# Kernel tuning notes

Hardware: AMD Instinct MI355X
Metric: run time of the kernel (lower is better)

Reference implementation:

```python
import jax, jax.numpy as jnp
import numpy as np

E = 512   # embed_dim
H = 8     # num_heads
B = 64    # num graphs
N = 255   # nodes per graph (equal counts -> padded mask is all-true)


def setup_inputs() -> dict:
    key = jax.random.key(0)
    ks = jax.random.split(key, 12)
    x = jax.random.normal(ks[0], (B * N, E), jnp.float32)
    metal_x = jax.random.normal(ks[1], (B, E), jnp.float32)
    batch = jnp.repeat(jnp.arange(B, dtype=jnp.int32), N)
    s = 1.0 / np.sqrt(E)
    def u(k, shape):
        return jax.random.uniform(k, shape, jnp.float32, -s, s)
    return {
        "x": x, "metal_x": metal_x, "batch": batch,
        "Wq": u(ks[2], (E, E)), "Wk": u(ks[3], (E, E)), "Wv": u(ks[4], (E, E)),
        "bq": u(ks[5], (E,)), "bk": u(ks[6], (E,)), "bv": u(ks[7], (E,)),
        "Wo": u(ks[8], (E, E)), "bo": u(ks[9], (E,)),
    }


def reference(x, metal_x, batch, Wq, Wk, Wv, bq, bk, bv, Wo, bo):
    # batch is sorted with equal per-graph counts, so the torch
    # pad_sequence([cat(metal_x[i], x[batch==i])]) construction is exactly a
    # reshape + concat, and key_padding_mask (~mask) is all-False.
    nb, e = metal_x.shape
    n = x.shape[0] // nb
    L = n + 1
    dh = e // H
    # value: [B, L, E] with the metal token at position 0
    value = jnp.concatenate([metal_x[:, None, :], x.reshape(nb, n, e)], axis=1)
    # key/query_sequential are identity; torch MHA in-projections (y = x W^T + b)
    q = value @ Wq.T + bq
    k = value @ Wk.T + bk
    v = value @ Wv.T + bv
    def heads(t):  # [B, L, E] -> [B, H, L, Dh]
        return t.reshape(nb, L, H, dh).transpose(0, 2, 1, 3)
    qh, kh, vh = heads(q), heads(k), heads(v)
    scale = 1.0 / jnp.sqrt(jnp.asarray(dh, q.dtype))
    scores = jnp.einsum('bhld,bhmd->bhlm', qh, kh) * scale
    attn = jax.nn.softmax(scores, axis=-1)
    oh = jnp.einsum('bhlm,bhmd->bhld', attn, vh)          # [B, H, L, Dh]
    out = oh.transpose(0, 2, 1, 3).reshape(nb, L, e) @ Wo.T + bo  # [B, L, E]
    # torch output is [L, B, E]; boolean indexing out[x_mask.T] iterates
    # row-major over (l, b): all graphs at node slot 1, then slot 2, ...
    out_lb = out.transpose(1, 0, 2)                        # [L, B, E]
    x_out = out_lb[1:].reshape(nb * n, e)
    metal_x_out = out_lb[0]                                # [B, E]
    return x_out, metal_x_out
```

## Files before the change

### kernel.cpp

```cpp
#include <hip/hip_runtime.h>
#include <stdint.h>


#define EMB    512
#define NH     8
#define NGR    64
#define SEQL   256
#define DHEAD  64
#define MROWS  16384

typedef __attribute__((ext_vector_type(4))) float f32x4;
typedef __attribute__((ext_vector_type(4))) short s16x4;
typedef __attribute__((ext_vector_type(8))) short s16x8;

__device__ __forceinline__ short f2bf(float f) {
  uint32_t u = __builtin_bit_cast(uint32_t, f);
  u += 0x7FFFu + ((u >> 16) & 1u);
  return (short)(u >> 16);
}

__device__ __forceinline__ f32x4 mfma16(s16x8 a, s16x8 b, f32x4 c) {
  return __builtin_amdgcn_mfma_f32_16x16x32_bf16(a, b, c, 0, 0, 0);
}

__device__ __forceinline__ void gload_lds16(const void* g, void* l) {
  __builtin_amdgcn_global_load_lds(
      (const __attribute__((address_space(1))) void*)g,
      (__attribute__((address_space(3))) void*)l, 16, 0, 0);
}


__global__ void pack_value(const float* __restrict__ x, const float* __restrict__ mx,
                           short* __restrict__ val) {
  int gid = blockIdx.x * 256 + threadIdx.x;
  int i = gid << 2;
  int row = i >> 9, col = i & 511;
  int b = row >> 8, l = row & 255;
  const float* src = l ? x  + ((size_t)(b * 255 + l - 1) << 9) + col
                       : mx + ((size_t)b << 9) + col;
  f32x4 f = *(const f32x4*)src;
  s16x4 o = { f2bf(f[0]), f2bf(f[1]), f2bf(f[2]), f2bf(f[3]) };
  *(s16x4*)(val + i) = o;
}

__global__ void pack_w(const float* __restrict__ Wq, const float* __restrict__ Wk,
                       const float* __restrict__ Wv, const float* __restrict__ Wo,
                       const float* __restrict__ bq, const float* __restrict__ bk,
                       const float* __restrict__ bv,
                       short* __restrict__ wqkv, short* __restrict__ wo,
                       float* __restrict__ bias_qkv) {
  int gid = blockIdx.x * 256 + threadIdx.x;
  int i = gid << 2;
  const float* src; short* dst;
  if (i < 786432) {
    int which = i >> 18, off = i & 262143;
    src = (which == 0 ? Wq : which == 1 ? Wk : Wv) + off;
    dst = wqkv + i;
  } else {
    int off = i - 786432;
    src = Wo + off; dst = wo + off;
  }
  f32x4 f = *(const f32x4*)src;
  s16x4 o = { f2bf(f[0]), f2bf(f[1]), f2bf(f[2]), f2bf(f[3]) };
  *(s16x4*)dst = o;
  if (gid < 1536)
    bias_qkv[gid] = gid < 512 ? bq[gid] : gid < 1024 ? bk[gid - 512] : bv[gid - 1024];
}

#define BM 128
#define BN 128
#define BK 32
#define NT 16

__global__ __launch_bounds__(256, 2) void gemm_bt(
    const short* __restrict__ A, const short* __restrict__ Bt,
    const float* __restrict__ bias, int mode,
    short* __restrict__ qb, short* __restrict__ kb, short* __restrict__ vb,
    float* __restrict__ outp) {
  __shared__ short As[3][BM * BK];
  __shared__ short Bs[3][BN * BK];
  const int tid = threadIdx.x;
  const int lane = tid & 63, wid = tid >> 6;
  const int wr = wid >> 1, wc = wid & 1;
  const int l15 = lane & 15, l4 = lane >> 4;
  const int bm = blockIdx.x * BM, bn = blockIdx.y * BN;

  auto STAGE = [&](int t, int b) {
    const int bk = t * BK;
#pragma unroll
    for (int i = 0; i < 2; ++i) {
      int idx = i * 256 + tid;
      int row = idx >> 2, cc = (idx & 3) * 8;
      gload_lds16(A + (size_t)(bm + row) * 512 + bk + cc, &As[b][idx * 8]);
      gload_lds16(Bt + (size_t)(bn + row) * 512 + bk + cc, &Bs[b][idx * 8]);
    }
  };

  f32x4 acc[4][4];
#pragma unroll
  for (int r = 0; r < 4; ++r)
#pragma unroll
    for (int c = 0; c < 4; ++c) acc[r][c] = (f32x4){0.f, 0.f, 0.f, 0.f};

  auto COMPUTE = [&](int b) {
    s16x8 af[4], bf[4];
#pragma unroll
    for (int r = 0; r < 4; ++r)
      af[r] = *(const s16x8*)(&As[b][(wr * 64 + r * 16 + l15) * BK + l4 * 8]);
#pragma unroll
    for (int c = 0; c < 4; ++c)
      bf[c] = *(const s16x8*)(&Bs[b][(wc * 64 + c * 16 + l15) * BK + l4 * 8]);
#pragma unroll
    for (int r = 0; r < 4; ++r)
#pragma unroll
      for (int c = 0; c < 4; ++c)
        acc[r][c] = mfma16(af[r], bf[c], acc[r][c]);
  };

  STAGE(0, 0);
  STAGE(1, 1);

  int cur = 0;
  for (int t = 0; t < NT - 1; ++t) {
    asm volatile("s_waitcnt vmcnt(4) lgkmcnt(0)" ::: "memory");
    __builtin_amdgcn_s_barrier();
    if (t < NT - 2) {
      int b2 = cur + 2; if (b2 >= 3) b2 -= 3;
      STAGE(t + 2, b2);
    }
    COMPUTE(cur);
    if (++cur == 3) cur = 0;
  }
  asm volatile("s_waitcnt vmcnt(0) lgkmcnt(0)" ::: "memory");
  __builtin_amdgcn_s_barrier();
  COMPUTE(cur);

#pragma unroll
  for (int r = 0; r < 4; ++r) {
    int row0 = bm + wr * 64 + r * 16 + l4 * 4;
#pragma unroll
    for (int c = 0; c < 4; ++c) {
      int col_g = bn + wc * 64 + c * 16 + l15;
      float bvv = bias[col_g];
#pragma unroll
      for (int j = 0; j < 4; ++j) {
        float v = acc[r][c][j] + bvv;
        int row = row0 + j;
        int b = row >> 8, lrow = row & 255;
        if (mode == 0) {
          int which = col_g >> 9, rem = col_g & 511;
          int h = rem >> 6, dh = rem & 63;
          size_t idx = ((size_t)((b * 8 + h) * 256 + lrow)) * 64 + dh;
          (which == 0 ? qb : which == 1 ? kb : vb)[idx] = f2bf(v);
        } else {
          size_t idx = (lrow == 0)
                         ? (size_t)16320 * 512 + (size_t)b * 512 + col_g
                         : ((size_t)(lrow - 1) * 64 + b) * 512 + col_g;
          outp[idx] = v;
        }
      }
    }
  }
}

#define VT_ROWB 544

__global__ __launch_bounds__(256, 2) void attn(
    const short* __restrict__ qb, const short* __restrict__ kb,
    const short* __restrict__ vb, short* __restrict__ attn_out) {
  __shared__ short Kl[256 * 64];
  __shared__ short VT[64 * 272];
  __shared__ short Pl[4][16 * 72];

  const int tid = threadIdx.x;
  const int lane = tid & 63, w = tid >> 6;
  const int l15 = lane & 15, l4 = lane >> 4;
  const int hb = blockIdx.x;
  const int bh = (hb & 7) * 64 + ((hb >> 3) >> 2);
  const int quarter = (hb >> 3) & 3;
  const size_t base = (size_t)bh * SEQL * DHEAD;

  {
    const char* kbytes = (const char*)(kb + base);
#pragma unroll
    for (int c = 0; c < 8; ++c) {
      int o = c * 4096 + tid * 16;
      int src = o ^ (((o >> 7) & 7) << 4);
      gload_lds16(kbytes + src, (char*)Kl + o);
    }
  }

  {
    int d0 = (tid & 7) * 8;
    int krow = tid >> 3;
#pragma unroll
    for (int step = 0; step < 8; ++step) {
      int key = step * 32 + krow;
      s16x8 vv = *(const s16x8*)(vb + base + (size_t)key * 64 + d0);
#pragma unroll
      for (int j = 0; j < 8; ++j) {
        int d = d0 + j;
        int off = d * VT_ROWB + ((key * 2) ^ ((d << 1) & 0x70));
        *(short*)((char*)VT + off) = vv[j];
      }
    }
  }

  const int q0 = quarter * 64 + w * 16;
  s16x8 qf[2];
#pragma unroll
  for (int kk = 0; kk < 2; ++kk)
    qf[kk] = *(const s16x8*)(qb + base + (size_t)(q0 + l15) * 64 + kk * 32 + l4 * 8);

  __syncthreads();

  f32x4 s[16];
#pragma unroll
  for (int ct = 0; ct < 16; ++ct) s[ct] = (f32x4){0.f, 0.f, 0.f, 0.f};

#pragma unroll
  for (int ct = 0; ct < 16; ++ct) {
    int rawb = (ct * 16 + l15) * 128 + l4 * 16;
    int swz = (l15 & 7) << 4;
    s16x8 kf0 = *(const s16x8*)((const char*)Kl + (rawb ^ swz));
    s16x8 kf1 = *(const s16x8*)((const char*)Kl + ((rawb + 64) ^ swz));
    s[ct] = mfma16(qf[0], kf0, s[ct]);
    s[ct] = mfma16(qf[1], kf1, s[ct]);
  }

  const float scale = 0.125f;
  float lsum[4];
#pragma unroll
  for (int j = 0; j < 4; ++j) {
    float m = -1e30f;
#pragma unroll
    for (int ct = 0; ct < 16; ++ct) m = fmaxf(m, s[ct][j]);
#pragma unroll
    for (int d = 1; d < 16; d <<= 1) m = fmaxf(m, __shfl_xor(m, d, 64));
    m *= scale;
    float ls = 0.f;
#pragma unroll
    for (int ct = 0; ct < 16; ++ct) {
      float p = __expf(s[ct][j] * scale - m);
      s[ct][j] = p;
      ls += p;
    }
#pragma unroll
    for (int d = 1; d < 16; d <<= 1) ls += __shfl_xor(ls, d, 64);
    lsum[j] = ls;
  }

  f32x4 o[4];
#pragma unroll
  for (int jt = 0; jt < 4; ++jt) o[jt] = (f32x4){0.f, 0.f, 0.f, 0.f};

#pragma unroll
  for (int ck = 0; ck < 4; ++ck) {
#pragma unroll
    for (int c2 = 0; c2 < 4; ++c2)
#pragma unroll
      for (int j = 0; j < 4; ++j) {
        int q = l4 * 4 + j;
        int col = c2 * 16 + l15;
        Pl[w][q * 72 + col] = f2bf(s[ck * 4 + c2][j]);
      }
#pragma unroll
    for (int kk = 0; kk < 2; ++kk) {
      s16x8 pf = *(const s16x8*)(&Pl[w][l15 * 72 + kk * 32 + l4 * 8]);
#pragma unroll
      for (int jt = 0; jt < 4; ++jt) {
        int d = jt * 16 + l15;
        int k0 = ck * 64 + kk * 32 + l4 * 8;
        int off = d * VT_ROWB + ((k0 * 2) ^ ((d << 1) & 0x70));
        s16x8 vf = *(const s16x8*)((const char*)VT + off);
        o[jt] = mfma16(pf, vf, o[jt]);
      }
    }
  }

  const int b = bh >> 3, h = bh & 7;
#pragma unroll
  for (int jt = 0; jt < 4; ++jt)
#pragma unroll
    for (int j = 0; j < 4; ++j) {
      float val = o[jt][j] / lsum[j];
      int qrow = q0 + l4 * 4 + j;
      int d = jt * 16 + l15;
      attn_out[(size_t)(b * 256 + qrow) * 512 + h * 64 + d] = f2bf(val);
    }
}


extern "C" void kernel_launch(void* const* d_in, const int* in_sizes, int n_in,
                              void* d_out, int out_size, void* d_ws, size_t ws_size,
                              hipStream_t stream) {
  (void)in_sizes; (void)n_in; (void)out_size; (void)ws_size;
  const float* x  = (const float*)d_in[0];
  const float* mx = (const float*)d_in[1];
  const float* Wq = (const float*)d_in[3];
  const float* Wk = (const float*)d_in[4];
  const float* Wv = (const float*)d_in[5];
  const float* bq = (const float*)d_in[6];
  const float* bk = (const float*)d_in[7];
  const float* bv = (const float*)d_in[8];
  const float* Wo = (const float*)d_in[9];
  const float* bo = (const float*)d_in[10];
  float* out = (float*)d_out;

  char* ws = (char*)d_ws;
  short* value = (short*)(ws);
  short* wqkv  = (short*)(ws + 16777216);
  short* wo    = (short*)(ws + 18350080);
  float* biasq = (float*)(ws + 18874368);
  short* qbuf  = (short*)(ws + 18880512);
  short* kbuf  = (short*)(ws + 35657728);
  short* vbuf  = (short*)(ws + 52434944);
  short* attn_o = value;

  pack_value<<<8192, 256, 0, stream>>>(x, mx, value);
  pack_w<<<1024, 256, 0, stream>>>(Wq, Wk, Wv, Wo, bq, bk, bv, wqkv, wo, biasq);
  gemm_bt<<<dim3(128, 12), 256, 0, stream>>>(value, wqkv, biasq, 0,
                                             qbuf, kbuf, vbuf, nullptr);
  attn<<<2048, 256, 0, stream>>>(qbuf, kbuf, vbuf, attn_o);
  gemm_bt<<<dim3(128, 4), 256, 0, stream>>>(attn_o, wo, bo, 1,
                                            nullptr, nullptr, nullptr, out);
}
```

Before: 184.5 us.

## Alias K and transposed V in one LDS buffer to raise attention occupancy

The attention kernel now keeps K and the transposed V in a single 32 KB shared buffer instead of two separate arrays. V is held in registers while QK^T runs, then written into the reused buffer after a barrier. The unpadded V row stride of 512 bytes is applied in both the transposed-V stores and the reads. Cutting LDS use is meant to let three blocks run per CU (launch bounds raised to 3), and s_setprio is raised around the MFMA loops. The cost is an extra barrier, 64 more live VGPRs for V during QK^T, and possible bank conflicts from dropping the V row padding.

```diff
diff --git a/kernel.cpp b/kernel.cpp
--- a/kernel.cpp
+++ b/kernel.cpp
@@ -163,13 +163,11 @@
   }
 }
 
-#define VT_ROWB 544
-
-__global__ __launch_bounds__(256, 2) void attn(
+
+__global__ __launch_bounds__(256, 3) void attn(
     const short* __restrict__ qb, const short* __restrict__ kb,
     const short* __restrict__ vb, short* __restrict__ attn_out) {
-  __shared__ short Kl[256 * 64];
-  __shared__ short VT[64 * 272];
+  __shared__ char KV[32768];
   __shared__ short Pl[4][16 * 72];
 
   const int tid = threadIdx.x;
@@ -186,25 +184,16 @@
     for (int c = 0; c < 8; ++c) {
       int o = c * 4096 + tid * 16;
       int src = o ^ (((o >> 7) & 7) << 4);
-      gload_lds16(kbytes + src, (char*)Kl + o);
-    }
-  }
-
-  {
-    int d0 = (tid & 7) * 8;
-    int krow = tid >> 3;
-#pragma unroll
-    for (int step = 0; step < 8; ++step) {
-      int key = step * 32 + krow;
-      s16x8 vv = *(const s16x8*)(vb + base + (size_t)key * 64 + d0);
-#pragma unroll
-      for (int j = 0; j < 8; ++j) {
-        int d = d0 + j;
-        int off = d * VT_ROWB + ((key * 2) ^ ((d << 1) & 0x70));
-        *(short*)((char*)VT + off) = vv[j];
-      }
-    }
-  }
+      gload_lds16(kbytes + src, KV + o);
+    }
+  }
+
+  const int d0 = (tid & 7) * 8;
+  const int krow = tid >> 3;
+  s16x8 vv[8];
+#pragma unroll
+  for (int step = 0; step < 8; ++step)
+    vv[step] = *(const s16x8*)(vb + base + (size_t)(step * 32 + krow) * 64 + d0);
 
   const int q0 = quarter * 64 + w * 16;
   s16x8 qf[2];
@@ -218,14 +207,29 @@
 #pragma unroll
   for (int ct = 0; ct < 16; ++ct) s[ct] = (f32x4){0.f, 0.f, 0.f, 0.f};
 
+  __builtin_amdgcn_s_setprio(1);
 #pragma unroll
   for (int ct = 0; ct < 16; ++ct) {
     int rawb = (ct * 16 + l15) * 128 + l4 * 16;
     int swz = (l15 & 7) << 4;
-    s16x8 kf0 = *(const s16x8*)((const char*)Kl + (rawb ^ swz));
-    s16x8 kf1 = *(const s16x8*)((const char*)Kl + ((rawb + 64) ^ swz));
+    s16x8 kf0 = *(const s16x8*)(KV + (rawb ^ swz));
+    s16x8 kf1 = *(const s16x8*)(KV + ((rawb + 64) ^ swz));
     s[ct] = mfma16(qf[0], kf0, s[ct]);
     s[ct] = mfma16(qf[1], kf1, s[ct]);
+  }
+  __builtin_amdgcn_s_setprio(0);
+
+  __syncthreads();
+
+#pragma unroll
+  for (int step = 0; step < 8; ++step) {
+    int key = step * 32 + krow;
+#pragma unroll
+    for (int j = 0; j < 8; ++j) {
+      int d = d0 + j;
+      int off = d * 512 + ((key * 2) ^ ((d << 1) & 0x70));
+      *(short*)(KV + off) = vv[step][j];
+    }
   }
 
   const float scale = 0.125f;
@@ -249,6 +253,8 @@
     for (int d = 1; d < 16; d <<= 1) ls += __shfl_xor(ls, d, 64);
     lsum[j] = ls;
   }
+
+  __syncthreads();
 
   f32x4 o[4];
 #pragma unroll
@@ -264,6 +270,7 @@
         int col = c2 * 16 + l15;
         Pl[w][q * 72 + col] = f2bf(s[ck * 4 + c2][j]);
       }
+    __builtin_amdgcn_s_setprio(1);
 #pragma unroll
     for (int kk = 0; kk < 2; ++kk) {
       s16x8 pf = *(const s16x8*)(&Pl[w][l15 * 72 + kk * 32 + l4 * 8]);
@@ -271,11 +278,12 @@
       for (int jt = 0; jt < 4; ++jt) {
         int d = jt * 16 + l15;
         int k0 = ck * 64 + kk * 32 + l4 * 8;
-        int off = d * VT_ROWB + ((k0 * 2) ^ ((d << 1) & 0x70));
-        s16x8 vf = *(const s16x8*)((const char*)VT + off);
+        int off = d * 512 + ((k0 * 2) ^ ((d << 1) & 0x70));
+        s16x8 vf = *(const s16x8*)(KV + off);
         o[jt] = mfma16(pf, vf, o[jt]);
       }
     }
+    __builtin_amdgcn_s_setprio(0);
   }
 
   const int b = bh >> 3, h = bh & 7;
```

New measurement: 189.4 us. 1.03x slower.
